# Optimization experiments

Hardware: AMD Instinct MI355X
Metric: run time of the kernel (lower is better)

The kernel has to match this reference:

```python
import jax, jax.numpy as jnp
import numpy as np

B, S, I, H = 64, 512, 512, 1024

def setup_inputs() -> dict:
    key = jax.random.key(0)
    k1, k2, k3, k4, k5 = jax.random.split(key, 5)
    bound = 1.0 / np.sqrt(H)  # PyTorch RNNCell init scale (values only; distribution irrelevant for correctness)
    return {
        "x_in": jax.random.normal(k1, (B, S, I), dtype=jnp.float32),
        "W_ih": jax.random.uniform(k2, (H, I), dtype=jnp.float32, minval=-bound, maxval=bound),
        "W_hh": jax.random.uniform(k3, (H, H), dtype=jnp.float32, minval=-bound, maxval=bound),
        "b_ih": jax.random.uniform(k4, (H,), dtype=jnp.float32, minval=-bound, maxval=bound),
        "b_hh": jax.random.uniform(k5, (H,), dtype=jnp.float32, minval=-bound, maxval=bound),
    }

def reference(x_in, W_ih, W_hh, b_ih, b_hh):
    # batch_first=True: x_in is (B, S, I). Permute to time-major (S, B, I).
    x_tm = jnp.transpose(x_in, (1, 0, 2))
    # Precompute input projections for all timesteps in one big GEMM: (S, B, H)
    x_proj = jnp.einsum("sbi,hi->sbh", x_tm, W_ih) + b_ih + b_hh
    h0 = jnp.zeros((x_in.shape[0], W_hh.shape[0]), dtype=x_in.dtype)

    def step(h, xp_t):
        h_new = jnp.tanh(xp_t + h @ W_hh.T)
        return h_new, h_new

    _, hiddens = jax.lax.scan(step, h0, x_proj)  # (S, B, H)
    return jnp.transpose(hiddens, (1, 0, 2))  # back to (B, S, H)
```

## Files before the change

kernel.cpp:

```cpp
#include <hip/hip_runtime.h>
#include <hip/hip_bf16.h>
#include <math.h>

#define B_ 64
#define S_ 512
#define I_ 512
#define H_ 1024

typedef __attribute__((ext_vector_type(8))) short short8;
typedef __attribute__((ext_vector_type(4))) short short4v;
typedef __attribute__((ext_vector_type(4))) float f32x4;

__device__ inline short bf16bits(float f) {
    __hip_bfloat16 h = __float2bfloat16(f);
    return __builtin_bit_cast(short, h);
}

#define BM 128
#define BN 128
#define BK 32
#define LDT 40

__global__ __launch_bounds__(256) void xproj_gemm(const float* __restrict__ X,
                                                  const float* __restrict__ Wih,
                                                  const float* __restrict__ bih,
                                                  const float* __restrict__ bhh,
                                                  float* __restrict__ out) {
    __shared__ __hip_bfloat16 sA[BM * LDT];
    __shared__ __hip_bfloat16 sB[BN * LDT];
    const int tid  = threadIdx.x;
    const int m0   = blockIdx.x * BM;
    const int n0   = blockIdx.y * BN;
    const int wave = tid >> 6;
    const int lane = tid & 63;
    const int quad = lane >> 4;
    const int l16  = lane & 15;
    const int wm   = (wave >> 1) * 64;
    const int wn   = (wave & 1) * 64;

    f32x4 acc[4][4] = {};

    for (int k0 = 0; k0 < I_; k0 += BK) {
#pragma unroll
        for (int i = 0; i < 4; ++i) {
            int idx = tid + i * 256;
            int r   = idx >> 3;
            int c4  = idx & 7;
            f32x4 a = *reinterpret_cast<const f32x4*>(X   + (size_t)(m0 + r) * I_ + k0 + c4 * 4);
            f32x4 b = *reinterpret_cast<const f32x4*>(Wih + (size_t)(n0 + r) * I_ + k0 + c4 * 4);
            short4v ap, bp;
            ap[0] = bf16bits(a[0]); ap[1] = bf16bits(a[1]); ap[2] = bf16bits(a[2]); ap[3] = bf16bits(a[3]);
            bp[0] = bf16bits(b[0]); bp[1] = bf16bits(b[1]); bp[2] = bf16bits(b[2]); bp[3] = bf16bits(b[3]);
            int off = r * LDT + c4 * 4;
            *reinterpret_cast<short4v*>(&sA[off]) = ap;
            *reinterpret_cast<short4v*>(&sB[off]) = bp;
        }
        __syncthreads();

        short8 af[4], bf[4];
#pragma unroll
        for (int mt = 0; mt < 4; ++mt)
            af[mt] = *reinterpret_cast<const short8*>(&sA[(wm + mt * 16 + l16) * LDT + quad * 8]);
#pragma unroll
        for (int nt = 0; nt < 4; ++nt)
            bf[nt] = *reinterpret_cast<const short8*>(&sB[(wn + nt * 16 + l16) * LDT + quad * 8]);
#pragma unroll
        for (int mt = 0; mt < 4; ++mt)
#pragma unroll
            for (int nt = 0; nt < 4; ++nt)
                acc[mt][nt] = __builtin_amdgcn_mfma_f32_16x16x32_bf16(af[mt], bf[nt], acc[mt][nt], 0, 0, 0);
        __syncthreads();
    }

#pragma unroll
    for (int mt = 0; mt < 4; ++mt) {
#pragma unroll
        for (int nt = 0; nt < 4; ++nt) {
            int gm = m0 + wm + mt * 16 + quad * 4;
            int gn = n0 + wn + nt * 16 + l16;
            float bias = bih[gn] + bhh[gn];
#pragma unroll
            for (int r = 0; r < 4; ++r)
                out[(size_t)(gm + r) * H_ + gn] = acc[mt][nt][r] + bias;
        }
    }
}

#define WLD 1032

__global__ __launch_bounds__(256) void rnn_steps(const float* __restrict__ Whh,
                                                 float* __restrict__ out,
                                                 unsigned short* __restrict__ hbuf,
                                                 unsigned int* __restrict__ cnt) {
    __shared__ __hip_bfloat16 Wl[16 * WLD];
    __shared__ float red[4][16][17];
    const int tid  = threadIdx.x;
    const int bid  = blockIdx.x;
    const int g    = bid >> 6;
    const int jblk = bid & 63;
    const int j0   = jblk * 16;
    const int b0   = g * 16;
    const int wave = tid >> 6;
    const int lane = tid & 63;
    const int quad = lane >> 4;
    const int l16  = lane & 15;
    const int m    = tid >> 4;
    const int n    = tid & 15;

    for (int idx = tid; idx < 16 * 256; idx += 256) {
        int r  = idx >> 8;
        int c4 = idx & 255;
        f32x4 w = *reinterpret_cast<const f32x4*>(Whh + (size_t)(j0 + r) * H_ + c4 * 4);
        short4v wp;
        wp[0] = bf16bits(w[0]); wp[1] = bf16bits(w[1]); wp[2] = bf16bits(w[2]); wp[3] = bf16bits(w[3]);
        *reinterpret_cast<short4v*>(&Wl[r * WLD + c4 * 4]) = wp;
    }
    __syncthreads();

    const size_t orow = (size_t)(b0 + m) * S_ * H_ + (j0 + n);
    unsigned int* mycnt = cnt + g * 32;

    for (int t = 0; t < S_; ++t) {
        float xp = __builtin_nontemporal_load(out + orow + (size_t)t * H_);
        float s = 0.f;

        if (t > 0) {
            if (tid == 0) {
                const unsigned int target = (unsigned int)t * 64u;
                int guard = 0;
                while (__hip_atomic_load(mycnt, __ATOMIC_RELAXED, __HIP_MEMORY_SCOPE_AGENT) < target) {
                    __builtin_amdgcn_s_sleep(1);
                    if (++guard > 1000000) break;
                }
                (void)__hip_atomic_load(mycnt, __ATOMIC_ACQUIRE, __HIP_MEMORY_SCOPE_AGENT);
            }
            __syncthreads();

            const unsigned short* hprev = hbuf + (size_t)((t - 1) & 1) * (B_ * H_);
            f32x4 acc = {0.f, 0.f, 0.f, 0.f};
            const int kbase = wave * 256;
#pragma unroll
            for (int i = 0; i < 8; ++i) {
                int k = kbase + i * 32 + quad * 8;
                short8 av = *reinterpret_cast<const short8*>(hprev + (size_t)(b0 + l16) * H_ + k);
                short8 bv = *reinterpret_cast<const short8*>(&Wl[l16 * WLD + k]);
                acc = __builtin_amdgcn_mfma_f32_16x16x32_bf16(av, bv, acc, 0, 0, 0);
            }
#pragma unroll
            for (int r = 0; r < 4; ++r)
                red[wave][quad * 4 + r][l16] = acc[r];
            __syncthreads();

            s = red[0][m][n] + red[1][m][n] + red[2][m][n] + red[3][m][n];
        }

        float val = tanhf(xp + s);
        __builtin_nontemporal_store(val, out + orow + (size_t)t * H_);

        float nb = __shfl_xor(val, 1, 64);
        unsigned int pair = ((unsigned int)(unsigned short)bf16bits(nb) << 16)
                          | (unsigned int)(unsigned short)bf16bits(val);
        if ((n & 1) == 0) {
            unsigned int* dst = (unsigned int*)(hbuf + (size_t)(t & 1) * (B_ * H_)
                                                + (size_t)(b0 + m) * H_ + (j0 + n));
            __hip_atomic_store(dst, pair, __ATOMIC_RELAXED, __HIP_MEMORY_SCOPE_AGENT);
        }
        __syncthreads();

        if (t < S_ - 1 && tid == 0) {
            __hip_atomic_fetch_add(mycnt, 1u, __ATOMIC_RELAXED, __HIP_MEMORY_SCOPE_AGENT);
        }
    }
}

extern "C" void kernel_launch(void* const* d_in, const int* in_sizes, int n_in,
                              void* d_out, int out_size, void* d_ws, size_t ws_size,
                              hipStream_t stream) {
    const float* x   = (const float*)d_in[0];
    const float* Wih = (const float*)d_in[1];
    const float* Whh = (const float*)d_in[2];
    const float* bih = (const float*)d_in[3];
    const float* bhh = (const float*)d_in[4];
    float* out = (float*)d_out;

    unsigned int* cnt = (unsigned int*)d_ws;
    unsigned short* hbuf = (unsigned short*)((char*)d_ws + 1024);

    hipMemsetAsync(d_ws, 0, 1024, stream);

    dim3 gA(256, 8);
    xproj_gemm<<<gA, 256, 0, stream>>>(x, Wih, bih, bhh, out);
    rnn_steps<<<256, 256, 0, stream>>>(Whh, out, hbuf, cnt);
}
```

Baseline: 2.316 ms.

## Replace shared atomic counter barrier with per-wave step flags polled by a wave

Swaps the per-group fetch_add counter, where 64 blocks contend on one word, for per-wave flag words that each wave stores with the step index after draining its h stores. Wave 0 of every block polls all 256 flags of its group in parallel and uses __all to decide when to proceed. The end-of-step __syncthreads is dropped and the flag is published before the large output store, so the critical path to the next step is shorter. The catch is more polling traffic, and correctness now relies on the vmcnt wait ordering the h stores ahead of the flag store.

```diff
diff --git a/kernel.cpp b/kernel.cpp
--- a/kernel.cpp
+++ b/kernel.cpp
@@ -91,7 +91,7 @@
 __global__ __launch_bounds__(256) void rnn_steps(const float* __restrict__ Whh,
                                                  float* __restrict__ out,
                                                  unsigned short* __restrict__ hbuf,
-                                                 unsigned int* __restrict__ cnt) {
+                                                 unsigned int* __restrict__ flags) {
     __shared__ __hip_bfloat16 Wl[16 * WLD];
     __shared__ float red[4][16][17];
     const int tid  = threadIdx.x;
@@ -118,21 +118,27 @@
     __syncthreads();
 
     const size_t orow = (size_t)(b0 + m) * S_ * H_ + (j0 + n);
-    unsigned int* mycnt = cnt + g * 32;
+    unsigned int* fgrp = flags + g * 256;
+    unsigned int* myflag = fgrp + jblk * 4 + wave;
 
     for (int t = 0; t < S_; ++t) {
         float xp = __builtin_nontemporal_load(out + orow + (size_t)t * H_);
         float s = 0.f;
 
         if (t > 0) {
-            if (tid == 0) {
-                const unsigned int target = (unsigned int)t * 64u;
+            if (wave == 0) {
+                const unsigned int target = (unsigned int)t;
+                const unsigned int* fl = fgrp + lane * 4;
                 int guard = 0;
-                while (__hip_atomic_load(mycnt, __ATOMIC_RELAXED, __HIP_MEMORY_SCOPE_AGENT) < target) {
-                    __builtin_amdgcn_s_sleep(1);
-                    if (++guard > 1000000) break;
-                }
-                (void)__hip_atomic_load(mycnt, __ATOMIC_ACQUIRE, __HIP_MEMORY_SCOPE_AGENT);
+                bool ok;
+                do {
+                    unsigned int f0 = __hip_atomic_load(fl + 0, __ATOMIC_RELAXED, __HIP_MEMORY_SCOPE_AGENT);
+                    unsigned int f1 = __hip_atomic_load(fl + 1, __ATOMIC_RELAXED, __HIP_MEMORY_SCOPE_AGENT);
+                    unsigned int f2 = __hip_atomic_load(fl + 2, __ATOMIC_RELAXED, __HIP_MEMORY_SCOPE_AGENT);
+                    unsigned int f3 = __hip_atomic_load(fl + 3, __ATOMIC_RELAXED, __HIP_MEMORY_SCOPE_AGENT);
+                    ok = (f0 >= target) & (f1 >= target) & (f2 >= target) & (f3 >= target);
+                } while (!__all(ok) && ++guard < 2000000);
+                (void)__hip_atomic_load(fl, __ATOMIC_ACQUIRE, __HIP_MEMORY_SCOPE_AGENT);
             }
             __syncthreads();
 
@@ -155,21 +161,22 @@
         }
 
         float val = tanhf(xp + s);
+
+        if (t < S_ - 1) {
+            float nb = __shfl_xor(val, 1, 64);
+            unsigned int pair = ((unsigned int)(unsigned short)bf16bits(nb) << 16)
+                              | (unsigned int)(unsigned short)bf16bits(val);
+            if ((n & 1) == 0) {
+                unsigned int* dst = (unsigned int*)(hbuf + (size_t)(t & 1) * (B_ * H_)
+                                                    + (size_t)(b0 + m) * H_ + (j0 + n));
+                __hip_atomic_store(dst, pair, __ATOMIC_RELAXED, __HIP_MEMORY_SCOPE_AGENT);
+            }
+            asm volatile("s_waitcnt vmcnt(0)" ::: "memory");
+            if (lane == 0)
+                __hip_atomic_store(myflag, (unsigned int)(t + 1), __ATOMIC_RELAXED, __HIP_MEMORY_SCOPE_AGENT);
+        }
+
         __builtin_nontemporal_store(val, out + orow + (size_t)t * H_);
-
-        float nb = __shfl_xor(val, 1, 64);
-        unsigned int pair = ((unsigned int)(unsigned short)bf16bits(nb) << 16)
-                          | (unsigned int)(unsigned short)bf16bits(val);
-        if ((n & 1) == 0) {
-            unsigned int* dst = (unsigned int*)(hbuf + (size_t)(t & 1) * (B_ * H_)
-                                                + (size_t)(b0 + m) * H_ + (j0 + n));
-            __hip_atomic_store(dst, pair, __ATOMIC_RELAXED, __HIP_MEMORY_SCOPE_AGENT);
-        }
-        __syncthreads();
-
-        if (t < S_ - 1 && tid == 0) {
-            __hip_atomic_fetch_add(mycnt, 1u, __ATOMIC_RELAXED, __HIP_MEMORY_SCOPE_AGENT);
-        }
     }
 }
 
@@ -183,12 +190,12 @@
     const float* bhh = (const float*)d_in[4];
     float* out = (float*)d_out;
 
-    unsigned int* cnt = (unsigned int*)d_ws;
-    unsigned short* hbuf = (unsigned short*)((char*)d_ws + 1024);
-
-    hipMemsetAsync(d_ws, 0, 1024, stream);
+    unsigned int* flags = (unsigned int*)d_ws;
+    unsigned short* hbuf = (unsigned short*)((char*)d_ws + 4096);
+
+    hipMemsetAsync(d_ws, 0, 4096, stream);
 
     dim3 gA(256, 8);
     xproj_gemm<<<gA, 256, 0, stream>>>(x, Wih, bih, bhh, out);
-    rnn_steps<<<256, 256, 0, stream>>>(Whh, out, hbuf, cnt);
-}
+    rnn_steps<<<256, 256, 0, stream>>>(Whh, out, hbuf, flags);
+}
```

Result: slower. 3.814 ms (+64.7%).
